# Performance work log

Hardware: AMD Instinct MI355X
Metric: run time of the kernel (lower is better)

## Reference

```python
import jax, jax.numpy as jnp
import numpy as np

BATCH = 1024
H = 1024  # input_size == hidden_size (forced by h0 = z.repeat)
STEPS = 4


def _uniform(key, shape, bound):
    return jax.random.uniform(key, shape, jnp.float32, -bound, bound)


def setup_inputs() -> dict:
    key = jax.random.key(0)
    ks = jax.random.split(key, 12)
    bound = 1.0 / np.sqrt(H)  # PyTorch LSTM/Linear default init range
    return {
        "z": jax.random.normal(ks[0], (BATCH, H), jnp.float32),
        # LSTM layer 0 (gate order: i, f, g, o)
        "W_ih0": _uniform(ks[1], (4 * H, H), bound),
        "W_hh0": _uniform(ks[2], (4 * H, H), bound),
        "b_ih0": _uniform(ks[3], (4 * H,), bound),
        "b_hh0": _uniform(ks[4], (4 * H,), bound),
        # LSTM layer 1
        "W_ih1": _uniform(ks[5], (4 * H, H), bound),
        "W_hh1": _uniform(ks[6], (4 * H, H), bound),
        "b_ih1": _uniform(ks[7], (4 * H,), bound),
        "b_hh1": _uniform(ks[8], (4 * H,), bound),
        # Output linear
        "W_lin": _uniform(ks[9], (H, H), bound),
        "b_lin": _uniform(ks[10], (H,), bound),
    }


def _lstm_cell(x, h, c, W_ih, W_hh, b_ih, b_hh):
    # PyTorch LSTM cell: gates = x W_ih^T + h W_hh^T + b_ih + b_hh, order i,f,g,o
    gates = x @ W_ih.T + h @ W_hh.T + (b_ih + b_hh)
    i, f, g, o = jnp.split(gates, 4, axis=-1)
    c_new = jax.nn.sigmoid(f) * c + jax.nn.sigmoid(i) * jnp.tanh(g)
    h_new = jax.nn.sigmoid(o) * jnp.tanh(c_new)
    return h_new, c_new


def reference(z, W_ih0, W_hh0, b_ih0, b_hh0, W_ih1, W_hh1, b_ih1, b_hh1, W_lin, b_lin):
    # init_hidden: both layers' h and c start as z; input each step is the constant z
    def step(carry, _):
        h0, c0, h1, c1 = carry
        h0, c0 = _lstm_cell(z, h0, c0, W_ih0, W_hh0, b_ih0, b_hh0)
        h1, c1 = _lstm_cell(h0, h1, c1, W_ih1, W_hh1, b_ih1, b_hh1)
        return (h0, c0, h1, c1), h1

    init = (z, z, z, z)
    _, outs = jax.lax.scan(step, init, None, length=STEPS)  # [4, B, H]
    feat = jnp.transpose(outs, (1, 0, 2))  # [B, 4, H]
    return feat @ W_lin.T + b_lin
```

## Files before the change

kernel.cpp:

```cpp
#include <hip/hip_runtime.h>
#include <hip/hip_bf16.h>
#include <cstdint>
#include <cstddef>


typedef __bf16 bf16_t;
typedef __bf16 bf16x8 __attribute__((ext_vector_type(8)));
typedef __bf16 bf16x4 __attribute__((ext_vector_type(4)));
typedef float f32x4 __attribute__((ext_vector_type(4)));

__device__ __forceinline__ void gload_lds16(const bf16_t* g, bf16_t* l) {
    __builtin_amdgcn_global_load_lds(
        (const __attribute__((address_space(1))) void*)g,
        (__attribute__((address_space(3))) void*)l,
        16, 0, 0);
}

__device__ __forceinline__ float sigmoid_f(float x) {
    return 1.f / (1.f + __expf(-x));
}
__device__ __forceinline__ float tanh_fast(float x) {
    const float t = __expf(2.f * x);
    return 1.f - 2.f / (t + 1.f);
}

struct Job {
    const bf16_t* A;
    const bf16_t* B;
    const float*  add;
    const float*  bias;
    float*        c;
    bf16_t*       h1;
    bf16_t*       h2;
    float*        C;
    int lda, K, h1s, h2s, mode;
};

__global__ __launch_bounds__(256, 2) void fused_multi(Job j0, Job j1, Job j2, int n0, int n01)
{
    __shared__ __align__(16) char smem[65536];
    bf16_t* lsA = (bf16_t*)smem;
    bf16_t* lsB = (bf16_t*)(smem + 16384);
    float*  gsm = (float*)smem;

    const int bid = blockIdx.x;
    Job ja; int local, n;
    if (bid < n0)        { ja = j0; local = bid;       n = n0; }
    else if (bid < n01)  { ja = j1; local = bid - n0;  n = n01 - n0; }
    else                 { ja = j2; local = bid - n01; n = (int)gridDim.x - n01; }

    const int q    = n >> 3;
    const int tile = (local & 7) * q + (local >> 3);
    const int bcol = (tile >> 3) * 128;
    const int brow = (tile & 7) * 128;

    const int tid  = threadIdx.x;
    const int lane = tid & 63;
    const int wave = tid >> 6;
    const int wm = (wave >> 1) * 64;
    const int wn = (wave & 1) * 64;

    const int srow = lane >> 3;
    const int ssw  = ((lane & 7) ^ srow) * 8;
    const int ch0  = wave * 4;
    const int nkt  = ja.K >> 6;

    const int fr  = lane & 15;
    const int g8  = (lane >> 4) * 8;
    const int rsw = (fr & 7) * 8;

    f32x4 acc[4][4] = {};

    auto stage = [&](int buf, int ktel) {
#pragma unroll
        for (int it = 0; it < 4; ++it) {
            const int ch = ch0 + it;
            const int row = ch * 8 + srow;
            gload_lds16(ja.A + (size_t)(brow + row) * ja.lda + ktel + ssw, &lsA[buf * 16384 + ch * 512]);
            gload_lds16(ja.B + (size_t)(bcol + row) * ja.K   + ktel + ssw, &lsB[buf * 16384 + ch * 512]);
        }
    };

    stage(0, 0);
    __syncthreads();

    for (int kt = 0; kt < nkt; ++kt) {
        const int buf = kt & 1;
        if (kt + 1 < nkt) stage(buf ^ 1, (kt + 1) << 6);
#pragma unroll
        for (int kk = 0; kk < 2; ++kk) {
            const int ko = (kk * 32 + g8) ^ rsw;
            bf16x8 af[4], bfv[4];
#pragma unroll
            for (int m = 0; m < 4; ++m)
                af[m] = *(const bf16x8*)&lsA[buf * 16384 + (wm + m * 16 + fr) * 64 + ko];
#pragma unroll
            for (int nn = 0; nn < 4; ++nn)
                bfv[nn] = *(const bf16x8*)&lsB[buf * 16384 + (wn + nn * 16 + fr) * 64 + ko];
#pragma unroll
            for (int m = 0; m < 4; ++m)
#pragma unroll
                for (int nn = 0; nn < 4; ++nn)
                    acc[m][nn] = __builtin_amdgcn_mfma_f32_16x16x32_bf16(af[m], bfv[nn], acc[m][nn], 0, 0, 0);
        }
        __syncthreads();
    }

    const int cr = (lane >> 4) * 4;
    const int cc = lane & 15;

    if (ja.mode == 1) {
#pragma unroll
        for (int nn = 0; nn < 4; ++nn) {
            const int col = bcol + wn + nn * 16 + cc;
            const float bv = ja.bias ? ja.bias[col] : 0.f;
#pragma unroll
            for (int m = 0; m < 4; ++m) {
                const int row0 = brow + wm + m * 16 + cr;
#pragma unroll
                for (int r = 0; r < 4; ++r)
                    ja.C[(size_t)(row0 + r) * 4096 + col] = acc[m][nn][r] + bv;
            }
        }
        return;
    }

#pragma unroll
    for (int nn = 0; nn < 4; ++nn)
#pragma unroll
        for (int m = 0; m < 4; ++m)
#pragma unroll
            for (int r = 0; r < 4; ++r) {
                const int row = wm + m * 16 + cr + r;
                const int col = wn + nn * 16 + cc;
                gsm[row * 128 + (col ^ (((row >> 2) & 1) << 4))] = acc[m][nn][r];
            }
    __syncthreads();

#pragma unroll
    for (int p = 0; p < 16; ++p) {
        const int idx = p * 256 + tid;
        const int rl = idx >> 5;
        const int nn = idx & 31;
        float4 gv = *(const float4*)&gsm[rl * 128 + ((nn * 4) ^ (((rl >> 2) & 1) << 4))];
        const int grow = brow + rl;
        const int j0c = bcol + nn * 4;
        if (ja.add) {
            const float4 av = *(const float4*)&ja.add[(size_t)grow * 4096 + j0c];
            gv.x += av.x; gv.y += av.y; gv.z += av.z; gv.w += av.w;
        }
        if (ja.bias) {
            const float4 bv = *(const float4*)&ja.bias[j0c];
            gv.x += bv.x; gv.y += bv.y; gv.z += bv.z; gv.w += bv.w;
        }
        const int ng = j0c >> 2;
        const size_t ci = (size_t)grow * 1024 + ng;
        const float cn = sigmoid_f(gv.y) * ja.c[ci] + sigmoid_f(gv.x) * tanh_fast(gv.z);
        const float hh = sigmoid_f(gv.w) * tanh_fast(cn);
        ja.c[ci] = cn;
        const bf16_t hb = (bf16_t)hh;
        ja.h1[(size_t)grow * ja.h1s + ng] = hb;
        if (ja.h2) ja.h2[(size_t)grow * ja.h2s + ng] = hb;
    }
}

__global__ __launch_bounds__(256) void prep_all(
    const float* __restrict__ z,
    const float4* __restrict__ Wih0, const float4* __restrict__ Whh0,
    const float4* __restrict__ Wih1, const float4* __restrict__ Whh1,
    const float4* __restrict__ Wlin,
    const float* __restrict__ bih0, const float* __restrict__ bhh0,
    const float* __restrict__ bih1, const float* __restrict__ bhh1,
    bf16x4* __restrict__ Wih0R, bf16x4* __restrict__ Whh0R, bf16x4* __restrict__ Wsum0R,
    bf16x4* __restrict__ WcatR1, bf16x4* __restrict__ Wlinb,
    bf16_t* __restrict__ zb, bf16_t* __restrict__ X0,
    float* __restrict__ c0, float* __restrict__ c1,
    float* __restrict__ b0R, float* __restrict__ b1R)
{
    const int t = blockIdx.x * 256 + threadIdx.x;
    if (t < 1048576) {
        const int j = t >> 8, col = t & 255;
        const int g = j & 3, nn = j >> 2;
        const int src = (g * 1024 + nn) * 256 + col;
        const float4 a = Wih0[src];
        const float4 b = Whh0[src];
        bf16x4 va = {(bf16_t)a.x, (bf16_t)a.y, (bf16_t)a.z, (bf16_t)a.w};
        bf16x4 vb = {(bf16_t)b.x, (bf16_t)b.y, (bf16_t)b.z, (bf16_t)b.w};
        bf16x4 vs = {(bf16_t)(a.x + b.x), (bf16_t)(a.y + b.y),
                     (bf16_t)(a.z + b.z), (bf16_t)(a.w + b.w)};
        Wih0R[t] = va; Whh0R[t] = vb; Wsum0R[t] = vs;
    } else if (t < 2097152) {
        const int i = t - 1048576;
        const int j = i >> 8, col = i & 255;
        const int g = j & 3, nn = j >> 2;
        const int src = (g * 1024 + nn) * 256 + col;
        const float4 a = Wih1[src];
        const float4 b = Whh1[src];
        bf16x4 va = {(bf16_t)a.x, (bf16_t)a.y, (bf16_t)a.z, (bf16_t)a.w};
        bf16x4 vb = {(bf16_t)b.x, (bf16_t)b.y, (bf16_t)b.z, (bf16_t)b.w};
        WcatR1[j * 512 + col]       = va;
        WcatR1[j * 512 + 256 + col] = vb;
    } else if (t < 2359296) {
        const int i = t - 2097152;
        const float4 a = Wlin[i];
        bf16x4 v = {(bf16_t)a.x, (bf16_t)a.y, (bf16_t)a.z, (bf16_t)a.w};
        Wlinb[i] = v;
    } else if (t < 2621440) {
        const int i = t - 2359296;
        const int b = i >> 8, n4 = i & 255;
        const float4 v = ((const float4*)z)[i];
        bf16x4 hv = {(bf16_t)v.x, (bf16_t)v.y, (bf16_t)v.z, (bf16_t)v.w};
        ((bf16x4*)zb)[i] = hv;
        *(bf16x4*)(X0 + (size_t)b * 2048 + 1024 + n4 * 4) = hv;
        ((float4*)c0)[i] = v;
        ((float4*)c1)[i] = v;
    } else if (t < 2622464) {
        const int nn = t - 2621440;
        float4 b0, b1;
        float* p0 = (float*)&b0; float* p1 = (float*)&b1;
#pragma unroll
        for (int g = 0; g < 4; ++g) {
            p0[g] = bih0[g * 1024 + nn] + bhh0[g * 1024 + nn];
            p1[g] = bih1[g * 1024 + nn] + bhh1[g * 1024 + nn];
        }
        ((float4*)b0R)[nn] = b0;
        ((float4*)b1R)[nn] = b1;
    }
}

extern "C" void kernel_launch(void* const* d_in, const int* in_sizes, int n_in,
                              void* d_out, int out_size, void* d_ws, size_t ws_size,
                              hipStream_t stream)
{
    const float* z     = (const float*)d_in[0];
    const float* W_ih0 = (const float*)d_in[1];
    const float* W_hh0 = (const float*)d_in[2];
    const float* b_ih0 = (const float*)d_in[3];
    const float* b_hh0 = (const float*)d_in[4];
    const float* W_ih1 = (const float*)d_in[5];
    const float* W_hh1 = (const float*)d_in[6];
    const float* b_ih1 = (const float*)d_in[7];
    const float* b_hh1 = (const float*)d_in[8];
    const float* W_lin = (const float*)d_in[9];
    const float* b_lin = (const float*)d_in[10];
    float* out = (float*)d_out;

    char* ws = (char*)d_ws;
    const size_t MB = 1u << 20;
    bf16_t* WcatR1 = (bf16_t*)(ws);
    bf16_t* Whh0R  = (bf16_t*)(ws + 16 * MB);
    bf16_t* Wih0R  = (bf16_t*)(ws + 24 * MB);
    bf16_t* Wsum0R = (bf16_t*)(ws + 32 * MB);
    bf16_t* Wlinb  = (bf16_t*)(ws + 40 * MB);
    bf16_t* zb     = (bf16_t*)(ws + 42 * MB);
    bf16_t* Xbuf   = (bf16_t*)(ws + 44 * MB);
    float*  Gz0R   = (float*) (ws + 52 * MB);
    bf16_t* stash  = (bf16_t*)(ws + 68 * MB);
    float*  c0     = (float*) (ws + 76 * MB);
    float*  c1     = (float*) (ws + 80 * MB);
    float*  bias0R = (float*) (ws + 84 * MB);
    float*  bias1R = (float*) (ws + 84 * MB + 16384);
    bf16_t* X[2] = {Xbuf, Xbuf + (size_t)(1u << 21)};

    prep_all<<<10244, 256, 0, stream>>>(
        z, (const float4*)W_ih0, (const float4*)W_hh0,
        (const float4*)W_ih1, (const float4*)W_hh1, (const float4*)W_lin,
        b_ih0, b_hh0, b_ih1, b_hh1,
        (bf16x4*)Wih0R, (bf16x4*)Whh0R, (bf16x4*)Wsum0R,
        (bf16x4*)WcatR1, (bf16x4*)Wlinb,
        zb, X[0], c0, c1, bias0R, bias1R);

    Job empty = {};

    {
        Job gz = {};
        gz.A = zb; gz.lda = 1024; gz.B = Wih0R; gz.K = 1024;
        gz.bias = bias0R; gz.C = Gz0R; gz.mode = 1;
        Job f00 = {};
        f00.A = zb; f00.lda = 1024; f00.B = Wsum0R; f00.K = 1024;
        f00.bias = bias0R; f00.c = c0; f00.h1 = X[0]; f00.h1s = 2048; f00.mode = 0;
        fused_multi<<<512, 256, 0, stream>>>(gz, f00, empty, 256, 512);
    }

    for (int t = 0; t < 4; ++t) {
        const int p = t & 1;
        Job a0 = {};
        a0.A = X[p]; a0.lda = 2048; a0.B = WcatR1; a0.K = 2048;
        a0.bias = bias1R; a0.c = c1;
        a0.h1 = stash + (size_t)t * (1u << 20); a0.h1s = 1024;
        if (t < 3) { a0.h2 = X[p ^ 1] + 1024; a0.h2s = 2048; }
        a0.mode = 0;

        Job a1 = {};
        if (t < 3) {
            a1.A = X[p]; a1.lda = 2048; a1.B = Whh0R; a1.K = 1024;
            a1.add = Gz0R; a1.c = c0; a1.h1 = X[p ^ 1]; a1.h1s = 2048; a1.mode = 0;
        }

        Job lj = {};
        if (t >= 1) {
            lj.A = stash + (size_t)(t - 1) * (1u << 20); lj.lda = 1024;
            lj.B = Wlinb; lj.K = 1024; lj.bias = b_lin;
            lj.C = out + (size_t)(t - 1) * 1024; lj.mode = 1;
        }

        if (t == 0)      fused_multi<<<512, 256, 0, stream>>>(a0, a1, empty, 256, 512);
        else if (t < 3)  fused_multi<<<576, 256, 0, stream>>>(a0, a1, lj, 256, 512);
        else             fused_multi<<<320, 256, 0, stream>>>(a0, lj, empty, 256, 320);
    }

    {
        Job lj = {};
        lj.A = stash + (size_t)3 * (1u << 20); lj.lda = 1024;
        lj.B = Wlinb; lj.K = 1024; lj.bias = b_lin;
        lj.C = out + (size_t)3 * 1024; lj.mode = 1;
        fused_multi<<<64, 256, 0, stream>>>(lj, empty, empty, 64, 64);
    }
}
```

Before: 238.6 us.

## Split K across wave pairs with 512-thread blocks and interleave jobs per block

Blocks grow to 512 threads. Each pair of waves splits the 64-wide K chunk in half and the two partial accumulators are reduced through LDS before the epilogue. Jobs are interleaved across even and odd block ids, and the output-linear tail tiles are appended to odd blocks, so every step uses a uniform 512-block grid. This aims to raise MFMA occupancy and balance the mixed GEMM work, at the cost of extra LDS reduction traffic and extra barriers, including dummy syncs for idle tiles.

```diff
diff --git a/kernel.cpp b/kernel.cpp
--- a/kernel.cpp
+++ b/kernel.cpp
@@ -33,51 +33,45 @@
     bf16_t*       h1;
     bf16_t*       h2;
     float*        C;
-    int lda, K, h1s, h2s, mode;
+    int lda, K, h1s, h2s, mode, ntiles;
 };
 
-__global__ __launch_bounds__(256, 2) void fused_multi(Job j0, Job j1, Job j2, int n0, int n01)
+__device__ void run_tile(const Job& ja, int local, char* smem)
 {
-    __shared__ __align__(16) char smem[65536];
-    bf16_t* lsA = (bf16_t*)smem;
-    bf16_t* lsB = (bf16_t*)(smem + 16384);
-    float*  gsm = (float*)smem;
-
-    const int bid = blockIdx.x;
-    Job ja; int local, n;
-    if (bid < n0)        { ja = j0; local = bid;       n = n0; }
-    else if (bid < n01)  { ja = j1; local = bid - n0;  n = n01 - n0; }
-    else                 { ja = j2; local = bid - n01; n = (int)gridDim.x - n01; }
-
-    const int q    = n >> 3;
-    const int tile = (local & 7) * q + (local >> 3);
+    if (local >= ja.ntiles) { __syncthreads(); __syncthreads(); __syncthreads(); return; }
+    const int q    = ja.ntiles >> 2;
+    const int tile = (local & 3) * q + (local >> 2);
     const int bcol = (tile >> 3) * 128;
     const int brow = (tile & 7) * 128;
 
     const int tid  = threadIdx.x;
     const int lane = tid & 63;
     const int wave = tid >> 6;
-    const int wm = (wave >> 1) * 64;
-    const int wn = (wave & 1) * 64;
+    const int pair = wave >> 1;
+    const int h    = wave & 1;
+    const int wm   = (pair >> 1) * 64;
+    const int wn   = (pair & 1) * 64;
 
     const int srow = lane >> 3;
     const int ssw  = ((lane & 7) ^ srow) * 8;
-    const int ch0  = wave * 4;
     const int nkt  = ja.K >> 6;
 
     const int fr  = lane & 15;
     const int g8  = (lane >> 4) * 8;
     const int rsw = (fr & 7) * 8;
+    const int ko  = (h * 32 + g8) ^ rsw;
 
     f32x4 acc[4][4] = {};
 
     auto stage = [&](int buf, int ktel) {
-#pragma unroll
-        for (int it = 0; it < 4; ++it) {
-            const int ch = ch0 + it;
+        bf16_t* lsA = (bf16_t*)(smem + buf * 32768);
+        bf16_t* lsB = lsA + 8192;
+#pragma unroll
+        for (int it = 0; it < 2; ++it) {
+            const int ch = wave * 2 + it;
             const int row = ch * 8 + srow;
-            gload_lds16(ja.A + (size_t)(brow + row) * ja.lda + ktel + ssw, &lsA[buf * 16384 + ch * 512]);
-            gload_lds16(ja.B + (size_t)(bcol + row) * ja.K   + ktel + ssw, &lsB[buf * 16384 + ch * 512]);
+            gload_lds16(ja.A + (size_t)(brow + row) * ja.lda + ktel + ssw, &lsA[ch * 512]);
+            gload_lds16(ja.B + (size_t)(bcol + row) * ja.K   + ktel + ssw, &lsB[ch * 512]);
         }
     };
 
@@ -87,59 +81,82 @@
     for (int kt = 0; kt < nkt; ++kt) {
         const int buf = kt & 1;
         if (kt + 1 < nkt) stage(buf ^ 1, (kt + 1) << 6);
-#pragma unroll
-        for (int kk = 0; kk < 2; ++kk) {
-            const int ko = (kk * 32 + g8) ^ rsw;
-            bf16x8 af[4], bfv[4];
-#pragma unroll
-            for (int m = 0; m < 4; ++m)
-                af[m] = *(const bf16x8*)&lsA[buf * 16384 + (wm + m * 16 + fr) * 64 + ko];
+        const bf16_t* lsA = (const bf16_t*)(smem + buf * 32768);
+        const bf16_t* lsB = lsA + 8192;
+        bf16x8 af[4], bfv[4];
+#pragma unroll
+        for (int m = 0; m < 4; ++m)
+            af[m] = *(const bf16x8*)&lsA[(wm + m * 16 + fr) * 64 + ko];
+#pragma unroll
+        for (int nn = 0; nn < 4; ++nn)
+            bfv[nn] = *(const bf16x8*)&lsB[(wn + nn * 16 + fr) * 64 + ko];
+#pragma unroll
+        for (int m = 0; m < 4; ++m)
 #pragma unroll
             for (int nn = 0; nn < 4; ++nn)
-                bfv[nn] = *(const bf16x8*)&lsB[buf * 16384 + (wn + nn * 16 + fr) * 64 + ko];
-#pragma unroll
-            for (int m = 0; m < 4; ++m)
-#pragma unroll
-                for (int nn = 0; nn < 4; ++nn)
-                    acc[m][nn] = __builtin_amdgcn_mfma_f32_16x16x32_bf16(af[m], bfv[nn], acc[m][nn], 0, 0, 0);
-        }
+                acc[m][nn] = __builtin_amdgcn_mfma_f32_16x16x32_bf16(af[m], bfv[nn], acc[m][nn], 0, 0, 0);
         __syncthreads();
     }
 
+    float* gsm = (float*)smem;
     const int cr = (lane >> 4) * 4;
     const int cc = lane & 15;
 
+    if (h == 0) {
+#pragma unroll
+        for (int nn = 0; nn < 4; ++nn)
+#pragma unroll
+            for (int m = 0; m < 4; ++m)
+#pragma unroll
+                for (int r = 0; r < 4; ++r) {
+                    const int row = wm + m * 16 + cr + r;
+                    const int col = wn + nn * 16 + cc;
+                    gsm[row * 128 + (col ^ (((row >> 2) & 1) << 4))] = acc[m][nn][r];
+                }
+    }
+    __syncthreads();
+
     if (ja.mode == 1) {
-#pragma unroll
-        for (int nn = 0; nn < 4; ++nn) {
-            const int col = bcol + wn + nn * 16 + cc;
-            const float bv = ja.bias ? ja.bias[col] : 0.f;
-#pragma unroll
-            for (int m = 0; m < 4; ++m) {
-                const int row0 = brow + wm + m * 16 + cr;
-#pragma unroll
-                for (int r = 0; r < 4; ++r)
-                    ja.C[(size_t)(row0 + r) * 4096 + col] = acc[m][nn][r] + bv;
+        if (h == 1) {
+#pragma unroll
+            for (int nn = 0; nn < 4; ++nn) {
+                const int col = wn + nn * 16 + cc;
+                const int gcol = bcol + col;
+                const float bv = ja.bias ? ja.bias[gcol] : 0.f;
+#pragma unroll
+                for (int m = 0; m < 4; ++m) {
+                    const int row0 = wm + m * 16 + cr;
+#pragma unroll
+                    for (int r = 0; r < 4; ++r) {
+                        const int row = row0 + r;
+                        const float v = gsm[row * 128 + (col ^ (((row >> 2) & 1) << 4))] + acc[m][nn][r];
+                        ja.C[(size_t)(brow + row) * 4096 + gcol] = v + bv;
+                    }
+                }
             }
         }
+        __syncthreads();
         return;
     }
 
-#pragma unroll
-    for (int nn = 0; nn < 4; ++nn)
-#pragma unroll
-        for (int m = 0; m < 4; ++m)
-#pragma unroll
-            for (int r = 0; r < 4; ++r) {
-                const int row = wm + m * 16 + cr + r;
-                const int col = wn + nn * 16 + cc;
-                gsm[row * 128 + (col ^ (((row >> 2) & 1) << 4))] = acc[m][nn][r];
-            }
+    if (h == 1) {
+#pragma unroll
+        for (int nn = 0; nn < 4; ++nn)
+#pragma unroll
+            for (int m = 0; m < 4; ++m)
+#pragma unroll
+                for (int r = 0; r < 4; ++r) {
+                    const int row = wm + m * 16 + cr + r;
+                    const int col = wn + nn * 16 + cc;
+                    const int a = row * 128 + (col ^ (((row >> 2) & 1) << 4));
+                    gsm[a] += acc[m][nn][r];
+                }
+    }
     __syncthreads();
 
 #pragma unroll
-    for (int p = 0; p < 16; ++p) {
-        const int idx = p * 256 + tid;
+    for (int p = 0; p < 8; ++p) {
+        const int idx = p * 512 + tid;
         const int rl = idx >> 5;
         const int nn = idx & 31;
         float4 gv = *(const float4*)&gsm[rl * 128 + ((nn * 4) ^ (((rl >> 2) & 1) << 4))];
@@ -162,6 +179,21 @@
         ja.h1[(size_t)grow * ja.h1s + ng] = hb;
         if (ja.h2) ja.h2[(size_t)grow * ja.h2s + ng] = hb;
     }
+    __syncthreads();
+}
+
+__global__ __launch_bounds__(512, 4) void fused_multi(Job je, Job jo, Job jt, int tailStart)
+{
+    __shared__ __align__(16) char smem[65536];
+    const int bid = blockIdx.x;
+    if (jo.ntiles == 0) {
+        run_tile(je, bid, smem);
+        return;
+    }
+    const bool even = !(bid & 1);
+    run_tile(even ? je : jo, bid >> 1, smem);
+    if (!even && jt.ntiles > 0 && bid >= tailStart)
+        run_tile(jt, (bid - tailStart) >> 1, smem);
 }
 
 __global__ __launch_bounds__(256) void prep_all(
@@ -275,11 +307,12 @@
     {
         Job gz = {};
         gz.A = zb; gz.lda = 1024; gz.B = Wih0R; gz.K = 1024;
-        gz.bias = bias0R; gz.C = Gz0R; gz.mode = 1;
+        gz.bias = bias0R; gz.C = Gz0R; gz.mode = 1; gz.ntiles = 256;
         Job f00 = {};
         f00.A = zb; f00.lda = 1024; f00.B = Wsum0R; f00.K = 1024;
-        f00.bias = bias0R; f00.c = c0; f00.h1 = X[0]; f00.h1s = 2048; f00.mode = 0;
-        fused_multi<<<512, 256, 0, stream>>>(gz, f00, empty, 256, 512);
+        f00.bias = bias0R; f00.c = c0; f00.h1 = X[0]; f00.h1s = 2048;
+        f00.mode = 0; f00.ntiles = 256;
+        fused_multi<<<512, 512, 0, stream>>>(gz, f00, empty, 1 << 30);
     }
 
     for (int t = 0; t < 4; ++t) {
@@ -289,31 +322,34 @@
         a0.bias = bias1R; a0.c = c1;
         a0.h1 = stash + (size_t)t * (1u << 20); a0.h1s = 1024;
         if (t < 3) { a0.h2 = X[p ^ 1] + 1024; a0.h2s = 2048; }
-        a0.mode = 0;
+        a0.mode = 0; a0.ntiles = 256;
 
         Job a1 = {};
         if (t < 3) {
             a1.A = X[p]; a1.lda = 2048; a1.B = Whh0R; a1.K = 1024;
-            a1.add = Gz0R; a1.c = c0; a1.h1 = X[p ^ 1]; a1.h1s = 2048; a1.mode = 0;
+            a1.add = Gz0R; a1.c = c0; a1.h1 = X[p ^ 1]; a1.h1s = 2048;
+            a1.mode = 0; a1.ntiles = 256;
+        } else {
+            a1.A = stash + (size_t)2 * (1u << 20); a1.lda = 1024;
+            a1.B = Wlinb; a1.K = 1024; a1.bias = b_lin;
+            a1.C = out + (size_t)2 * 1024; a1.mode = 1; a1.ntiles = 64;
         }
 
         Job lj = {};
-        if (t >= 1) {
+        if (t == 1 || t == 2) {
             lj.A = stash + (size_t)(t - 1) * (1u << 20); lj.lda = 1024;
             lj.B = Wlinb; lj.K = 1024; lj.bias = b_lin;
-            lj.C = out + (size_t)(t - 1) * 1024; lj.mode = 1;
-        }
-
-        if (t == 0)      fused_multi<<<512, 256, 0, stream>>>(a0, a1, empty, 256, 512);
-        else if (t < 3)  fused_multi<<<576, 256, 0, stream>>>(a0, a1, lj, 256, 512);
-        else             fused_multi<<<320, 256, 0, stream>>>(a0, lj, empty, 256, 320);
+            lj.C = out + (size_t)(t - 1) * 1024; lj.mode = 1; lj.ntiles = 64;
+        }
+
+        fused_multi<<<512, 512, 0, stream>>>(a0, a1, lj, 385);
     }
 
     {
         Job lj = {};
         lj.A = stash + (size_t)3 * (1u << 20); lj.lda = 1024;
         lj.B = Wlinb; lj.K = 1024; lj.bias = b_lin;
-        lj.C = out + (size_t)3 * 1024; lj.mode = 1;
-        fused_multi<<<64, 256, 0, stream>>>(lj, empty, empty, 64, 64);
-    }
-}
+        lj.C = out + (size_t)3 * 1024; lj.mode = 1; lj.ntiles = 64;
+        fused_multi<<<64, 512, 0, stream>>>(lj, empty, empty, 1 << 30);
+    }
+}
```

Result: slower. 418.7 us (+75.5%).
